# Performance work log

Hardware: AMD Instinct MI355X
Metric: run time of the kernel (lower is better)

The kernel has to match this reference:

```python
import jax, jax.numpy as jnp
import numpy as np

S = 1024          # num tokens (single prefill sequence)
H = 2880          # hidden_size
NH = 64           # num query heads
NKV = 8           # num kv heads
HD = 64           # head_dim
G = NH // NKV     # query heads per kv head
THETA = 10000.0
SCALE = HD ** -0.5


def _rope(x, positions):
    # neox-style rotary over full head_dim; x: [S, n_heads, HD]
    half = HD // 2
    inv_freq = 1.0 / (THETA ** (jnp.arange(half, dtype=jnp.float32) / half))
    ang = positions.astype(jnp.float32)[:, None] * inv_freq          # [S, half]
    cos = jnp.cos(ang)[:, None, :]
    sin = jnp.sin(ang)[:, None, :]
    x1, x2 = x[..., :half], x[..., half:]
    return jnp.concatenate([x1 * cos - x2 * sin, x2 * cos + x1 * sin], axis=-1)


def setup_inputs() -> dict:
    key = jax.random.key(0)
    k0, k1, k2, k3 = jax.random.split(key, 4)
    return {
        "positions": jnp.arange(S, dtype=jnp.int32),
        "hidden_states": jax.random.normal(k0, (S, H), dtype=jnp.float32),
        "qkv_w": jax.random.normal(k1, ((NH + 2 * NKV) * HD, H), dtype=jnp.float32) * 0.02,
        "o_w": jax.random.normal(k2, (H, NH * HD), dtype=jnp.float32) * 0.02,
        "sinks": jax.random.normal(k3, (NH,), dtype=jnp.float32),
    }


def reference(positions, hidden_states, qkv_w, o_w, sinks):
    # fused QKV projection (no bias, matching attention_bias=False)
    qkv = hidden_states @ qkv_w.T                                     # [S, 5120]
    q = qkv[:, : NH * HD].reshape(S, NH, HD)
    k = qkv[:, NH * HD : NH * HD + NKV * HD].reshape(S, NKV, HD)
    v = qkv[:, NH * HD + NKV * HD :].reshape(S, NKV, HD)

    # rotary on q and k (rotary_dim == head_dim)
    q = _rope(q, positions)
    k = _rope(k, positions)

    # GQA: group query heads by kv head -> [S, NKV, G, HD]
    qg = q.reshape(S, NKV, G, HD)

    logits = jnp.einsum("qghd,kgd->ghqk", qg, k) * SCALE              # [NKV, G, S, S]
    causal = positions[:, None] >= positions[None, :]                 # [S, S]
    logits = jnp.where(causal[None, None], logits, -jnp.inf)

    # attention sinks: per-head extra logit in the softmax denominator,
    # contributing no value vector.
    sink = sinks.reshape(NKV, G)[:, :, None, None]                    # [NKV, G, 1, 1]
    m = jnp.maximum(jnp.max(logits, axis=-1, keepdims=True), sink)
    p = jnp.exp(logits - m)                                           # [NKV, G, S, S]
    denom = jnp.sum(p, axis=-1, keepdims=True) + jnp.exp(sink - m)
    attn = jnp.einsum("ghqk,kgd->qghd", p / denom, v)                 # [S, NKV, G, HD]

    out = attn.reshape(S, NH * HD) @ o_w.T                            # [S, H]
    return out
```

## Files before the change

### kernel.cpp

```cpp
#include <hip/hip_runtime.h>
#include <hip/hip_bf16.h>
#include <math.h>

#define S_LEN 1024
#define HDIM  2880
#define NH    64
#define NKV   8
#define HD    64
#define QKV_N ((NH + 2*NKV) * HD)
#define O_K   (NH * HD)
#define SCALE 0.125f

typedef _Float16 f16x8 __attribute__((ext_vector_type(8)));
typedef _Float16 f16x4 __attribute__((ext_vector_type(4)));
typedef float    f32x4 __attribute__((ext_vector_type(4)));

__device__ __forceinline__ void cvt4(const float* __restrict__ s,
                                     _Float16* __restrict__ d, int i) {
    const float4 v = ((const float4*)s)[i];
    f16x4 p;
    p[0] = (_Float16)v.x; p[1] = (_Float16)v.y;
    p[2] = (_Float16)v.z; p[3] = (_Float16)v.w;
    ((f16x4*)d)[i] = p;
}

__global__ __launch_bounds__(256) void cvt_f32_f16(const float* __restrict__ src,
                                                   _Float16* __restrict__ dst, int n4) {
    const int stride = gridDim.x * blockDim.x;
    for (int i = blockIdx.x * blockDim.x + threadIdx.x; i < n4; i += stride)
        cvt4(src, dst, i);
}

__global__ __launch_bounds__(256) void cvt_all(const float* __restrict__ h,
                                               const float* __restrict__ qw,
                                               const float* __restrict__ ow,
                                               _Float16* __restrict__ dh,
                                               _Float16* __restrict__ dqw,
                                               _Float16* __restrict__ dow) {
    const int stride = gridDim.x * blockDim.x;
    const int t0 = blockIdx.x * blockDim.x + threadIdx.x;
    for (int i = t0; i < 737280;  i += stride) cvt4(h,  dh,  i);
    for (int i = t0; i < 3686400; i += stride) cvt4(qw, dqw, i);
    for (int i = t0; i < 2949120; i += stride) cvt4(ow, dow, i);
}

#define CSTR 68

#define DMA16(GP, LP) __builtin_amdgcn_global_load_lds( \
        (const __attribute__((address_space(1))) void*)(GP), \
        (__attribute__((address_space(3))) void*)(LP), 16, 0, 0)

template<typename CT>
__global__ __launch_bounds__(256) void gemm_ff(const _Float16* __restrict__ A,
                                               const _Float16* __restrict__ B,
                                               CT* __restrict__ C,
                                               int M, int N, int K) {
    __shared__ __align__(16) _Float16 sh[16384];

    const int tid  = threadIdx.x;
    const int lane = tid & 63;
    const int wave = tid >> 6;
    const int wr   = wave >> 1;
    const int wc   = wave & 1;
    const int quad = lane >> 4;
    const int fr   = lane & 15;
    const int ks   = quad * 8;
    const int row0 = blockIdx.y * 128;
    const int col0 = blockIdx.x * 128;

    const int klen   = K / (int)gridDim.z;
    const int kb     = (int)blockIdx.z * klen;
    const int nsteps = klen / 32;
    CT* Cp = C + (size_t)blockIdx.z * M * N;

    const int r0   = tid >> 2;
    const int ch   = (tid & 3) * 8;
    const int dst0 = (tid & ~63) * 8;

    const size_t aoff0 = (size_t)(row0 + r0)      * K;
    const size_t aoff1 = (size_t)(row0 + r0 + 64) * K;
    int bR0 = col0 + r0;      if (bR0 >= N) bR0 = N - 1;
    int bR1 = col0 + r0 + 64; if (bR1 >= N) bR1 = N - 1;
    const size_t boff0 = (size_t)bR0 * K;
    const size_t boff1 = (size_t)bR1 * K;

    f32x4 acc[4][4] = {};

    {
        const int kk = kb + ch;
        DMA16(A + aoff0 + kk, sh + dst0);
        DMA16(A + aoff1 + kk, sh + 2048 + dst0);
        DMA16(B + boff0 + kk, sh + 8192 + dst0);
        DMA16(B + boff1 + kk, sh + 8192 + 2048 + dst0);
    }

    for (int step = 0; step < nsteps; ++step) {
        const int cur = step & 1;
        _Float16* Acur = sh + cur * 4096;
        _Float16* Anxt = sh + (cur ^ 1) * 4096;
        _Float16* Bcur = sh + 8192 + cur * 4096;
        _Float16* Bnxt = sh + 8192 + (cur ^ 1) * 4096;

        __syncthreads();

        if (step + 1 < nsteps) {
            const int k1 = kb + (step + 1) * 32 + ch;
            DMA16(A + aoff0 + k1, Anxt + dst0);
            DMA16(A + aoff1 + k1, Anxt + 2048 + dst0);
            DMA16(B + boff0 + k1, Bnxt + dst0);
            DMA16(B + boff1 + k1, Bnxt + 2048 + dst0);
        }

        f16x8 af[4], bf[4];
#pragma unroll
        for (int mi = 0; mi < 4; ++mi)
            af[mi] = *(const f16x8*)&Acur[(wr * 64 + mi * 16 + fr) * 32 + ks];
#pragma unroll
        for (int ni = 0; ni < 4; ++ni)
            bf[ni] = *(const f16x8*)&Bcur[(wc * 64 + ni * 16 + fr) * 32 + ks];
#pragma unroll
        for (int mi = 0; mi < 4; ++mi)
#pragma unroll
            for (int ni = 0; ni < 4; ++ni)
                acc[mi][ni] = __builtin_amdgcn_mfma_f32_16x16x32_f16(
                    af[mi], bf[ni], acc[mi][ni], 0, 0, 0);
    }

#pragma unroll
    for (int p = 0; p < 2; ++p) {
        __syncthreads();
        if (wc == p) {
#pragma unroll
            for (int mi = 0; mi < 4; ++mi)
#pragma unroll
                for (int ni = 0; ni < 4; ++ni) {
                    const f32x4 v = acc[mi][ni];
#pragma unroll
                    for (int r = 0; r < 4; ++r)
                        sh[(wr * 64 + mi * 16 + quad * 4 + r) * CSTR + ni * 16 + fr] =
                            (_Float16)v[r];
                }
        }
        __syncthreads();
#pragma unroll
        for (int it = 0; it < 4; ++it) {
            const int id  = it * 256 + tid;
            const int row = id >> 3;
            const int chh = (id & 7) * 8;
            const int col = col0 + p * 64 + chh;
            if (col < N) {
                const f16x4 lo = *(const f16x4*)&sh[row * CSTR + chh];
                const f16x4 hi = *(const f16x4*)&sh[row * CSTR + chh + 4];
                if constexpr (sizeof(CT) == 2) {
                    f16x8 v;
                    v[0]=lo[0]; v[1]=lo[1]; v[2]=lo[2]; v[3]=lo[3];
                    v[4]=hi[0]; v[5]=hi[1]; v[6]=hi[2]; v[7]=hi[3];
                    *(f16x8*)&Cp[(size_t)(row0 + row) * N + col] = v;
                } else {
                    float4 v0 = make_float4((float)lo[0], (float)lo[1],
                                            (float)lo[2], (float)lo[3]);
                    float4 v1 = make_float4((float)hi[0], (float)hi[1],
                                            (float)hi[2], (float)hi[3]);
                    *(float4*)&Cp[(size_t)(row0 + row) * N + col]     = v0;
                    *(float4*)&Cp[(size_t)(row0 + row) * N + col + 4] = v1;
                }
            }
        }
    }
}

template<typename CT>
__global__ __launch_bounds__(256) void gemm_f16(const _Float16* __restrict__ A,
                                                const float* __restrict__ B,
                                                CT* __restrict__ C,
                                                int M, int N, int K) {
    __shared__ __align__(16) _Float16 sh[16384];

    const int tid  = threadIdx.x;
    const int lane = tid & 63;
    const int wave = tid >> 6;
    const int wr   = wave >> 1;
    const int wc   = wave & 1;
    const int quad = lane >> 4;
    const int fr   = lane & 15;
    const int ks   = quad * 8;
    const int row0 = blockIdx.y * 128;
    const int col0 = blockIdx.x * 128;

    const int klen   = K / (int)gridDim.z;
    const int kb     = (int)blockIdx.z * klen;
    const int nsteps = klen / 32;
    CT* Cp = C + (size_t)blockIdx.z * M * N;

    const int a_cbase0 = wave * 64;
    const int a_ci0 = a_cbase0 + lane;
    const int a_r0 = a_ci0 >> 2, a_ch0 = a_ci0 & 3;
    const int a_cbase1 = 256 + wave * 64;
    const int a_ci1 = a_cbase1 + lane;
    const int a_r1 = a_ci1 >> 2, a_ch1 = a_ci1 & 3;
    int b_r[4], b_ch[4];
#pragma unroll
    for (int it = 0; it < 4; ++it) {
        const int c4 = it * 256 + tid;
        b_r[it]  = c4 >> 3;
        b_ch[it] = (c4 & 7) << 2;
    }

    float4 breg[4];
    f32x4 acc[4][4] = {};

    {
        const _Float16* gp0 = A + (size_t)(row0 + a_r0) * K + kb + a_ch0 * 8;
        DMA16(gp0, sh + (size_t)a_cbase0 * 8);
        const _Float16* gp1 = A + (size_t)(row0 + a_r1) * K + kb + a_ch1 * 8;
        DMA16(gp1, sh + (size_t)a_cbase1 * 8);
#pragma unroll
        for (int it = 0; it < 4; ++it) {
            int brow = col0 + b_r[it];
            if (brow >= N) brow = N - 1;
            breg[it] = *(const float4*)&B[(size_t)brow * K + kb + b_ch[it]];
        }
        _Float16* Bs0 = sh + 8192;
#pragma unroll
        for (int it = 0; it < 4; ++it) {
            f16x4 p;
            p[0] = (_Float16)breg[it].x; p[1] = (_Float16)breg[it].y;
            p[2] = (_Float16)breg[it].z; p[3] = (_Float16)breg[it].w;
            *(f16x4*)&Bs0[b_r[it] * 32 + b_ch[it]] = p;
        }
    }

    for (int step = 0; step < nsteps; ++step) {
        const int cur = step & 1;
        const int nxt = cur ^ 1;
        _Float16* Acur = sh + cur * 4096;
        _Float16* Anxt = sh + nxt * 4096;
        _Float16* Bcur = sh + 8192 + cur * 4096;
        _Float16* Bnxt = sh + 8192 + nxt * 4096;

        __syncthreads();

        const bool more = (step + 1 < nsteps);
        if (more) {
            const int k1 = kb + (step + 1) * 32;
            const _Float16* gp0 = A + (size_t)(row0 + a_r0) * K + k1 + a_ch0 * 8;
            DMA16(gp0, Anxt + (size_t)a_cbase0 * 8);
            const _Float16* gp1 = A + (size_t)(row0 + a_r1) * K + k1 + a_ch1 * 8;
            DMA16(gp1, Anxt + (size_t)a_cbase1 * 8);
#pragma unroll
            for (int it = 0; it < 4; ++it) {
                int brow = col0 + b_r[it];
                if (brow >= N) brow = N - 1;
                breg[it] = *(const float4*)&B[(size_t)brow * K + k1 + b_ch[it]];
            }
        }

        f16x8 af[4], bfr[4];
#pragma unroll
        for (int mi = 0; mi < 4; ++mi)
            af[mi] = *(const f16x8*)&Acur[(wr * 64 + mi * 16 + fr) * 32 + ks];
#pragma unroll
        for (int ni = 0; ni < 4; ++ni)
            bfr[ni] = *(const f16x8*)&Bcur[(wc * 64 + ni * 16 + fr) * 32 + ks];
#pragma unroll
        for (int mi = 0; mi < 4; ++mi)
#pragma unroll
            for (int ni = 0; ni < 4; ++ni)
                acc[mi][ni] = __builtin_amdgcn_mfma_f32_16x16x32_f16(
                    af[mi], bfr[ni], acc[mi][ni], 0, 0, 0);

        if (more) {
#pragma unroll
            for (int it = 0; it < 4; ++it) {
                f16x4 p;
                p[0] = (_Float16)breg[it].x; p[1] = (_Float16)breg[it].y;
                p[2] = (_Float16)breg[it].z; p[3] = (_Float16)breg[it].w;
                *(f16x4*)&Bnxt[b_r[it] * 32 + b_ch[it]] = p;
            }
        }
    }

#pragma unroll
    for (int p = 0; p < 2; ++p) {
        __syncthreads();
        if (wc == p) {
#pragma unroll
            for (int mi = 0; mi < 4; ++mi)
#pragma unroll
                for (int ni = 0; ni < 4; ++ni) {
                    const f32x4 v = acc[mi][ni];
#pragma unroll
                    for (int r = 0; r < 4; ++r)
                        sh[(wr * 64 + mi * 16 + quad * 4 + r) * CSTR + ni * 16 + fr] =
                            (_Float16)v[r];
                }
        }
        __syncthreads();
#pragma unroll
        for (int it = 0; it < 4; ++it) {
            const int id  = it * 256 + tid;
            const int row = id >> 3;
            const int chh = (id & 7) * 8;
            const int col = col0 + p * 64 + chh;
            if (col < N) {
                const f16x4 lo = *(const f16x4*)&sh[row * CSTR + chh];
                const f16x4 hi = *(const f16x4*)&sh[row * CSTR + chh + 4];
                if constexpr (sizeof(CT) == 2) {
                    f16x8 v;
                    v[0]=lo[0]; v[1]=lo[1]; v[2]=lo[2]; v[3]=lo[3];
                    v[4]=hi[0]; v[5]=hi[1]; v[6]=hi[2]; v[7]=hi[3];
                    *(f16x8*)&Cp[(size_t)(row0 + row) * N + col] = v;
                } else {
                    float4 v0 = make_float4((float)lo[0], (float)lo[1],
                                            (float)lo[2], (float)lo[3]);
                    float4 v1 = make_float4((float)hi[0], (float)hi[1],
                                            (float)hi[2], (float)hi[3]);
                    *(float4*)&Cp[(size_t)(row0 + row) * N + col]     = v0;
                    *(float4*)&Cp[(size_t)(row0 + row) * N + col + 4] = v1;
                }
            }
        }
    }
}

__global__ __launch_bounds__(256) void rope_reduce(_Float16* __restrict__ parts,
                                                   int nsplit,
                                                   _Float16* __restrict__ vt,
                                                   const int* __restrict__ positions) {
    __shared__ float buf[QKV_N];
    const int s   = blockIdx.x;
    const int tid = threadIdx.x;
    const size_t PSTR = (size_t)S_LEN * QKV_N;

    for (int c = tid; c < QKV_N / 4; c += 256) {
        float4 a = make_float4(0.f, 0.f, 0.f, 0.f);
        for (int j = 0; j < nsplit; ++j) {
            const f16x4 v = ((const f16x4*)(parts + j * PSTR + (size_t)s * QKV_N))[c];
            a.x += (float)v[0]; a.y += (float)v[1];
            a.z += (float)v[2]; a.w += (float)v[3];
        }
        ((float4*)buf)[c] = a;
    }
    __syncthreads();

    const float pos = (float)positions[s];
    _Float16* orow = parts + (size_t)s * QKV_N;
    for (int w = tid; w < 72 * 32; w += 256) {
        const int h = w >> 5;
        const int t = w & 31;
        const float inv_freq = exp2f(-(float)t * (13.287712379549449f / 32.0f));
        const float ang = pos * inv_freq;
        float sn, cs;
        sincosf(ang, &sn, &cs);
        const float x1 = buf[h * 64 + t];
        const float x2 = buf[h * 64 + t + 32];
        orow[h * 64 + t]      = (_Float16)(x1 * cs - x2 * sn);
        orow[h * 64 + t + 32] = (_Float16)(x2 * cs + x1 * sn);
    }
    for (int c = tid; c < NKV * HD; c += 256)
        vt[(size_t)c * S_LEN + s] = (_Float16)buf[(NH + NKV) * HD + c];
}

__global__ __launch_bounds__(256) void o_reduce(const _Float16* __restrict__ parts,
                                                float* __restrict__ out,
                                                int n4, int nsplit) {
    const size_t PSTR = (size_t)S_LEN * HDIM;
    const int stride = gridDim.x * blockDim.x;
    for (int i = blockIdx.x * blockDim.x + threadIdx.x; i < n4; i += stride) {
        float4 a = make_float4(0.f, 0.f, 0.f, 0.f);
        for (int j = 0; j < nsplit; ++j) {
            const f16x4 v = ((const f16x4*)(parts + j * PSTR))[i];
            a.x += (float)v[0]; a.y += (float)v[1];
            a.z += (float)v[2]; a.w += (float)v[3];
        }
        ((float4*)out)[i] = a;
    }
}

#define LSTR 72
__global__ __launch_bounds__(256) void attn_mfma(const _Float16* __restrict__ qkv,
                                                 const _Float16* __restrict__ vt,
                                                 const float* __restrict__ sinks,
                                                 const int* __restrict__ positions,
                                                 _Float16* __restrict__ attn_out) {
    __shared__ __align__(16) _Float16 Ks[2][64 * LSTR];
    __shared__ __align__(16) _Float16 Vs[2][64 * LSTR];
    __shared__ __align__(16) _Float16 Ps[64 * LSTR];

    const int tid  = threadIdx.x;
    const int lane = tid & 63;
    const int wave = tid >> 6;
    const int fr   = lane & 15;
    const int quad = lane >> 4;
    const int ks8  = quad * 8;
    const int n    = blockIdx.x;
    const int qt   = (int)gridDim.y - 1 - (int)blockIdx.y;
    const int g    = n >> 3;

    int st_r[2], st_o[2];
#pragma unroll
    for (int it = 0; it < 2; ++it) {
        const int c = it * 256 + tid;
        st_r[it] = c >> 3;
        st_o[it] = (c & 7) * 8;
    }

    const _Float16* qrow = qkv + (size_t)(qt * 64 + wave * 16 + fr) * QKV_N + n * HD;
    const f16x8 a_q0 = *(const f16x8*)&qrow[ks8];
    const f16x8 a_q1 = *(const f16x8*)&qrow[32 + ks8];

    int pq[4];
#pragma unroll
    for (int r = 0; r < 4; ++r)
        pq[r] = positions[qt * 64 + wave * 16 + quad * 4 + r];

    const float sinkv = sinks[n];
    float m[4], l[4];
    f32x4 o[4] = {};
#pragma unroll
    for (int r = 0; r < 4; ++r) { m[r] = sinkv; l[r] = 1.0f; }

    f16x8 kreg[2], vreg[2];
    {
        const _Float16* Kg = qkv + (size_t)0 * QKV_N + NH * HD + g * HD;
        const _Float16* Vg = vt + (size_t)(g * HD) * S_LEN;
#pragma unroll
        for (int it = 0; it < 2; ++it) {
            kreg[it] = *(const f16x8*)&Kg[(size_t)st_r[it] * QKV_N + st_o[it]];
            vreg[it] = *(const f16x8*)&Vg[(size_t)st_r[it] * S_LEN + st_o[it]];
        }
#pragma unroll
        for (int it = 0; it < 2; ++it) {
            *(f16x8*)&Ks[0][st_r[it] * LSTR + st_o[it]] = kreg[it];
            *(f16x8*)&Vs[0][st_r[it] * LSTR + st_o[it]] = vreg[it];
        }
    }

    for (int kt = 0; kt <= qt; ++kt) {
        const int cur = kt & 1;
        const int nxt = cur ^ 1;
        __syncthreads();

        const bool more = (kt < qt);
        if (more) {
            const _Float16* Kg = qkv + (size_t)((kt + 1) * 64) * QKV_N + NH * HD + g * HD;
            const _Float16* Vg = vt + (size_t)(g * HD) * S_LEN + (kt + 1) * 64;
#pragma unroll
            for (int it = 0; it < 2; ++it) {
                kreg[it] = *(const f16x8*)&Kg[(size_t)st_r[it] * QKV_N + st_o[it]];
                vreg[it] = *(const f16x8*)&Vg[(size_t)st_r[it] * S_LEN + st_o[it]];
            }
        }

        f32x4 s[4] = {};
#pragma unroll
        for (int nt = 0; nt < 4; ++nt) {
            const f16x8 b0 = *(const f16x8*)&Ks[cur][(nt * 16 + fr) * LSTR + ks8];
            s[nt] = __builtin_amdgcn_mfma_f32_16x16x32_f16(a_q0, b0, s[nt], 0, 0, 0);
            const f16x8 b1 = *(const f16x8*)&Ks[cur][(nt * 16 + fr) * LSTR + 32 + ks8];
            s[nt] = __builtin_amdgcn_mfma_f32_16x16x32_f16(a_q1, b1, s[nt], 0, 0, 0);
        }

        const bool diag = (kt == qt);
        int pk[4];
        if (diag) {
#pragma unroll
            for (int nt = 0; nt < 4; ++nt) pk[nt] = positions[qt * 64 + nt * 16 + fr];
        }
#pragma unroll
        for (int nt = 0; nt < 4; ++nt)
#pragma unroll
            for (int r = 0; r < 4; ++r) {
                float sv = s[nt][r] * SCALE;
                if (diag && pk[nt] > pq[r]) sv = -3.0e38f;
                s[nt][r] = sv;
            }

#pragma unroll
        for (int r = 0; r < 4; ++r) {
            float tm = fmaxf(fmaxf(s[0][r], s[1][r]), fmaxf(s[2][r], s[3][r]));
            tm = fmaxf(tm, __shfl_xor(tm, 1, 64));
            tm = fmaxf(tm, __shfl_xor(tm, 2, 64));
            tm = fmaxf(tm, __shfl_xor(tm, 4, 64));
            tm = fmaxf(tm, __shfl_xor(tm, 8, 64));
            const float nm = fmaxf(m[r], tm);
            const float alpha = __expf(m[r] - nm);
            float rs = 0.0f;
#pragma unroll
            for (int nt = 0; nt < 4; ++nt) {
                const float p = __expf(s[nt][r] - nm);
                s[nt][r] = p;
                rs += p;
            }
            rs += __shfl_xor(rs, 1, 64);
            rs += __shfl_xor(rs, 2, 64);
            rs += __shfl_xor(rs, 4, 64);
            rs += __shfl_xor(rs, 8, 64);
            l[r] = l[r] * alpha + rs;
            m[r] = nm;
#pragma unroll
            for (int nt = 0; nt < 4; ++nt) o[nt][r] *= alpha;
        }

#pragma unroll
        for (int nt = 0; nt < 4; ++nt)
#pragma unroll
            for (int r = 0; r < 4; ++r)
                Ps[(wave * 16 + quad * 4 + r) * LSTR + nt * 16 + fr] = (_Float16)s[nt][r];
        __threadfence_block();

#pragma unroll
        for (int k2 = 0; k2 < 2; ++k2) {
            const f16x8 ap = *(const f16x8*)&Ps[(wave * 16 + fr) * LSTR + k2 * 32 + ks8];
#pragma unroll
            for (int nt = 0; nt < 4; ++nt) {
                const f16x8 bv = *(const f16x8*)&Vs[cur][(nt * 16 + fr) * LSTR + k2 * 32 + ks8];
                o[nt] = __builtin_amdgcn_mfma_f32_16x16x32_f16(ap, bv, o[nt], 0, 0, 0);
            }
        }

        if (more) {
#pragma unroll
            for (int it = 0; it < 2; ++it) {
                *(f16x8*)&Ks[nxt][st_r[it] * LSTR + st_o[it]] = kreg[it];
                *(f16x8*)&Vs[nxt][st_r[it] * LSTR + st_o[it]] = vreg[it];
            }
        }
    }

#pragma unroll
    for (int r = 0; r < 4; ++r) {
        const float inv = 1.0f / l[r];
        const size_t row = (size_t)(qt * 64 + wave * 16 + quad * 4 + r);
#pragma unroll
        for (int nt = 0; nt < 4; ++nt)
            attn_out[row * O_K + n * HD + nt * 16 + fr] = (_Float16)(o[nt][r] * inv);
    }
}

extern "C" void kernel_launch(void* const* d_in, const int* in_sizes, int n_in,
                              void* d_out, int out_size, void* d_ws, size_t ws_size,
                              hipStream_t stream) {
    const int*   positions = (const int*)d_in[0];
    const float* hidden    = (const float*)d_in[1];
    const float* qkv_w     = (const float*)d_in[2];
    const float* o_w       = (const float*)d_in[3];
    const float* sinks     = (const float*)d_in[4];
    float* out = (float*)d_out;

    const size_t n_hid  = (size_t)S_LEN * HDIM;
    const size_t n_qkv  = (size_t)S_LEN * QKV_N;
    const size_t n_attn = (size_t)S_LEN * O_K;
    const size_t n_vt   = (size_t)NKV * HD * S_LEN;
    const size_t n_out  = (size_t)S_LEN * HDIM;
    const size_t n_qw   = (size_t)QKV_N * HDIM;
    const size_t n_ow   = (size_t)HDIM * O_K;

    const int SP_Q = 3;
    const int SP_O = 4;

    const size_t need_full =
        (n_hid + SP_Q * n_qkv + n_attn + n_vt + n_qw + n_ow) * sizeof(_Float16);
    const size_t need_mid  = (n_hid + SP_Q * n_qkv + n_attn + n_vt) * sizeof(_Float16);

    if (ws_size >= need_full) {
        _Float16* hid_h  = (_Float16*)d_ws;
        _Float16* qkvp   = hid_h + n_hid;
        _Float16* attn_h = qkvp + SP_Q * n_qkv;
        _Float16* vt     = attn_h + n_attn;
        _Float16* qw_h   = vt + n_vt;
        _Float16* ow_h   = qw_h + n_qw;
        _Float16* opart  = qkvp;

        cvt_all<<<2048, 256, 0, stream>>>(hidden, qkv_w, o_w, hid_h, qw_h, ow_h);
        gemm_ff<_Float16><<<dim3(QKV_N / 128, S_LEN / 128, SP_Q), 256, 0, stream>>>(
            hid_h, qw_h, qkvp, S_LEN, QKV_N, HDIM);
        rope_reduce<<<S_LEN, 256, 0, stream>>>(qkvp, SP_Q, vt, positions);
        attn_mfma<<<dim3(NH, S_LEN / 64), 256, 0, stream>>>(qkvp, vt, sinks, positions, attn_h);
        gemm_ff<_Float16><<<dim3((HDIM + 127) / 128, S_LEN / 128, SP_O), 256, 0, stream>>>(
            attn_h, ow_h, opart, S_LEN, HDIM, O_K);
        o_reduce<<<1024, 256, 0, stream>>>(opart, out, (int)(n_out / 4), SP_O);
    } else if (ws_size >= need_mid) {
        _Float16* hid_h  = (_Float16*)d_ws;
        _Float16* qkvp   = hid_h + n_hid;
        _Float16* attn_h = qkvp + SP_Q * n_qkv;
        _Float16* vt     = attn_h + n_attn;
        _Float16* opart  = qkvp;

        cvt_f32_f16<<<512, 256, 0, stream>>>(hidden, hid_h, (int)(n_hid / 4));
        gemm_f16<_Float16><<<dim3(QKV_N / 128, S_LEN / 128, SP_Q), 256, 0, stream>>>(
            hid_h, qkv_w, qkvp, S_LEN, QKV_N, HDIM);
        rope_reduce<<<S_LEN, 256, 0, stream>>>(qkvp, SP_Q, vt, positions);
        attn_mfma<<<dim3(NH, S_LEN / 64), 256, 0, stream>>>(qkvp, vt, sinks, positions, attn_h);
        gemm_f16<_Float16><<<dim3((HDIM + 127) / 128, S_LEN / 128, SP_O), 256, 0, stream>>>(
            attn_h, o_w, opart, S_LEN, HDIM, O_K);
        o_reduce<<<1024, 256, 0, stream>>>(opart, out, (int)(n_out / 4), SP_O);
    } else {
        _Float16* hid_h  = (_Float16*)d_ws;
        _Float16* qkvp   = hid_h + n_hid;
        _Float16* attn_h = qkvp + n_qkv;
        _Float16* vt     = attn_h + n_attn;

        cvt_f32_f16<<<512, 256, 0, stream>>>(hidden, hid_h, (int)(n_hid / 4));
        gemm_f16<_Float16><<<dim3(QKV_N / 128, S_LEN / 128, 1), 256, 0, stream>>>(
            hid_h, qkv_w, qkvp, S_LEN, QKV_N, HDIM);
        rope_reduce<<<S_LEN, 256, 0, stream>>>(qkvp, 1, vt, positions);
        attn_mfma<<<dim3(NH, S_LEN / 64), 256, 0, stream>>>(qkvp, vt, sinks, positions, attn_h);
        gemm_f16<float><<<dim3((HDIM + 127) / 128, S_LEN / 128, 1), 256, 0, stream>>>(
            attn_h, o_w, out, S_LEN, HDIM, O_K);
    }
}
```

Measured before the change: 298.4 us.

## Add 256x256-tile eight-wave ping-pong GEMM for QKV and output projections

Introduces a new fp16 MFMA GEMM kernel with 256x256 block tiles and 512 threads. It uses direct global-to-LDS loads into double buffers with an XOR-swizzled layout, and interleaves quarter-tile MFMA phases with barriers and raised wave priority so that loads for the next K tile overlap compute. Both projection GEMMs in the full-workspace path now use it instead of the 128x128 kernel. The aim is more data reuse per block and fewer blocks. The cost is 128KB of LDS per block, which limits occupancy, and a grid of only a few hundred blocks, which may leave some CUs underused.

```diff
diff --git a/kernel.cpp b/kernel.cpp
--- a/kernel.cpp
+++ b/kernel.cpp
@@ -14,6 +14,15 @@
 typedef _Float16 f16x8 __attribute__((ext_vector_type(8)));
 typedef _Float16 f16x4 __attribute__((ext_vector_type(4)));
 typedef float    f32x4 __attribute__((ext_vector_type(4)));
+
+#define DMA16(GP, LP) __builtin_amdgcn_global_load_lds( \
+        (const __attribute__((address_space(1))) void*)(GP), \
+        (__attribute__((address_space(3))) void*)(LP), 16, 0, 0)
+
+#define BARRIER() __builtin_amdgcn_s_barrier()
+#define WAITV(n)  asm volatile("s_waitcnt vmcnt(" #n ")" ::: "memory")
+#define WAITL()   asm volatile("s_waitcnt lgkmcnt(0)" ::: "memory")
+#define SCHED0()  __builtin_amdgcn_sched_barrier(0)
 
 __device__ __forceinline__ void cvt4(const float* __restrict__ s,
                                      _Float16* __restrict__ d, int i) {
@@ -44,12 +53,177 @@
     for (int i = t0; i < 2949120; i += stride) cvt4(ow, dow, i);
 }
 
+__device__ __forceinline__ f16x8 lds_frag(const _Float16* base, int row, int kf) {
+    return *(const f16x8*)&base[row * 64 + (kf ^ ((row & 7) << 3))];
+}
+
+__device__ __forceinline__ void mfma_quad(f32x4 (&acc)[8][4], const f16x8 (&af)[4][2],
+                                          const f16x8 (&bf)[2][2], int mh, int nh) {
+    __builtin_amdgcn_s_setprio(1);
+#pragma unroll
+    for (int q4 = 0; q4 < 4; ++q4)
+#pragma unroll
+        for (int n2 = 0; n2 < 2; ++n2) {
+            f32x4 a = acc[mh * 4 + q4][nh * 2 + n2];
+            a = __builtin_amdgcn_mfma_f32_16x16x32_f16(af[q4][0], bf[n2][0], a, 0, 0, 0);
+            a = __builtin_amdgcn_mfma_f32_16x16x32_f16(af[q4][1], bf[n2][1], a, 0, 0, 0);
+            acc[mh * 4 + q4][nh * 2 + n2] = a;
+        }
+    __builtin_amdgcn_s_setprio(0);
+}
+
+__global__ __launch_bounds__(512, 2) void gemm_8p(const _Float16* __restrict__ A,
+                                                  const _Float16* __restrict__ B,
+                                                  _Float16* __restrict__ C,
+                                                  int M, int N, int K) {
+    __shared__ __align__(16) _Float16 sh[65536];
+
+    const int tid  = threadIdx.x;
+    const int lane = tid & 63;
+    const int wave = tid >> 6;
+    const int wr   = wave >> 2;
+    const int wc   = wave & 3;
+    const int quad = lane >> 4;
+    const int fr   = lane & 15;
+    const int row0 = blockIdx.y * 256;
+    const int col0 = blockIdx.x * 256;
+
+    const int klen = K / (int)gridDim.z;
+    const int kb   = (int)blockIdx.z * klen;
+    const int NT   = klen / 64;
+    _Float16* Cp = C + (size_t)blockIdx.z * M * N;
+
+    int    stDst[2];
+    size_t aOff[2][2], bOff[2][2];
+#pragma unroll
+    for (int r = 0; r < 2; ++r) {
+        const int c   = r * 512 + tid;
+        const int row = c >> 3;
+        const int sw  = ((c & 7) ^ (row & 7)) * 8;
+        stDst[r] = (c & ~63) * 8;
+#pragma unroll
+        for (int h = 0; h < 2; ++h) {
+            aOff[h][r] = (size_t)(row0 + h * 128 + row) * K + sw;
+            int br = col0 + h * 128 + row; if (br > N - 1) br = N - 1;
+            bOff[h][r] = (size_t)br * K + sw;
+        }
+    }
+    const _Float16* Ab = A + kb;
+    const _Float16* Bb = B + kb;
+
+#define STAGE2(GB, OFF, LB) do { \
+        DMA16((GB) + (OFF)[0], (LB) + stDst[0]); \
+        DMA16((GB) + (OFF)[1], (LB) + stDst[1]); } while (0)
+
+    f32x4 acc[8][4] = {};
+
+    STAGE2(Ab, aOff[0], sh);
+    STAGE2(Ab, aOff[1], sh + 8192);
+    STAGE2(Bb, bOff[0], sh + 32768);
+    STAGE2(Bb, bOff[1], sh + 32768 + 8192);
+    if (NT > 1) {
+        STAGE2(Ab + 64, aOff[0], sh + 16384);
+        STAGE2(Ab + 64, aOff[1], sh + 16384 + 8192);
+        WAITV(4);
+    } else {
+        WAITV(0);
+    }
+    BARRIER();
+
+    for (int t = 0; t < NT; ++t) {
+        _Float16* Ac = sh + ((t & 1) ? 16384 : 0);
+        _Float16* Bc = sh + 32768 + ((t & 1) ? 16384 : 0);
+        _Float16* Bn = sh + 32768 + ((t & 1) ? 0 : 16384);
+        const bool st1 = (t + 1 < NT);
+        const bool st2 = (t + 2 < NT);
+        const int  k1  = (t + 1) * 64;
+        const int  k2  = (t + 2) * 64;
+
+        f16x8 aF0[4][2], aF1[4][2], bF[2][2];
+
+#pragma unroll
+        for (int q4 = 0; q4 < 4; ++q4) {
+            const int row = wr * 128 + q4 * 16 + fr;
+            aF0[q4][0] = lds_frag(Ac, row, quad * 8);
+            aF0[q4][1] = lds_frag(Ac, row, 32 + quad * 8);
+        }
+#pragma unroll
+        for (int n2 = 0; n2 < 2; ++n2) {
+            const int row = wc * 64 + n2 * 16 + fr;
+            bF[n2][0] = lds_frag(Bc, row, quad * 8);
+            bF[n2][1] = lds_frag(Bc, row, 32 + quad * 8);
+        }
+        if (st1) STAGE2(Bb + k1, bOff[0], Bn);
+        BARRIER(); WAITL(); SCHED0();
+        mfma_quad(acc, aF0, bF, 0, 0);
+        BARRIER();
+
+#pragma unroll
+        for (int q4 = 0; q4 < 4; ++q4) {
+            const int row = wr * 128 + 64 + q4 * 16 + fr;
+            aF1[q4][0] = lds_frag(Ac, row, quad * 8);
+            aF1[q4][1] = lds_frag(Ac, row, 32 + quad * 8);
+        }
+        if (st1) STAGE2(Bb + k1, bOff[1], Bn + 8192);
+        BARRIER(); WAITL(); SCHED0();
+        mfma_quad(acc, aF1, bF, 1, 0);
+        BARRIER();
+
+#pragma unroll
+        for (int n2 = 0; n2 < 2; ++n2) {
+            const int row = wc * 64 + 32 + n2 * 16 + fr;
+            bF[n2][0] = lds_frag(Bc, row, quad * 8);
+            bF[n2][1] = lds_frag(Bc, row, 32 + quad * 8);
+        }
+        if (st2) STAGE2(Ab + k2, aOff[0], Ac);
+        BARRIER(); WAITL(); SCHED0();
+        mfma_quad(acc, aF1, bF, 1, 1);
+        BARRIER();
+
+        if (st2) {
+            STAGE2(Ab + k2, aOff[1], Ac + 8192);
+            WAITV(4);
+        } else {
+            WAITV(0);
+        }
+        BARRIER(); WAITL(); SCHED0();
+        mfma_quad(acc, aF0, bF, 0, 1);
+        BARRIER();
+    }
+
+    __syncthreads();
+    _Float16* cbuf = sh;
+#pragma unroll
+    for (int h = 0; h < 2; ++h) {
+        if (wr == h) {
+#pragma unroll
+            for (int mi = 0; mi < 8; ++mi)
+#pragma unroll
+                for (int ni = 0; ni < 4; ++ni) {
+                    const f32x4 v = acc[mi][ni];
+#pragma unroll
+                    for (int rr = 0; rr < 4; ++rr)
+                        cbuf[(mi * 16 + quad * 4 + rr) * 264 + wc * 64 + ni * 16 + fr] =
+                            (_Float16)v[rr];
+                }
+        }
+        __syncthreads();
+#pragma unroll
+        for (int u = 0; u < 8; ++u) {
+            const int c    = u * 512 + tid;
+            const int rowL = c >> 5;
+            const int ch   = (c & 31) * 8;
+            const int col  = col0 + ch;
+            if (col < N)
+                *(f16x8*)&Cp[(size_t)(row0 + h * 128 + rowL) * N + col] =
+                    *(const f16x8*)&cbuf[rowL * 264 + ch];
+        }
+        __syncthreads();
+    }
+#undef STAGE2
+}
+
 #define CSTR 68
-
-#define DMA16(GP, LP) __builtin_amdgcn_global_load_lds( \
-        (const __attribute__((address_space(1))) void*)(GP), \
-        (__attribute__((address_space(3))) void*)(LP), 16, 0, 0)
-
 template<typename CT>
 __global__ __launch_bounds__(256) void gemm_ff(const _Float16* __restrict__ A,
                                                const _Float16* __restrict__ B,
@@ -573,11 +747,11 @@
         _Float16* opart  = qkvp;
 
         cvt_all<<<2048, 256, 0, stream>>>(hidden, qkv_w, o_w, hid_h, qw_h, ow_h);
-        gemm_ff<_Float16><<<dim3(QKV_N / 128, S_LEN / 128, SP_Q), 256, 0, stream>>>(
+        gemm_8p<<<dim3(QKV_N / 256, S_LEN / 256, SP_Q), 512, 0, stream>>>(
             hid_h, qw_h, qkvp, S_LEN, QKV_N, HDIM);
         rope_reduce<<<S_LEN, 256, 0, stream>>>(qkvp, SP_Q, vt, positions);
         attn_mfma<<<dim3(NH, S_LEN / 64), 256, 0, stream>>>(qkvp, vt, sinks, positions, attn_h);
-        gemm_ff<_Float16><<<dim3((HDIM + 127) / 128, S_LEN / 128, SP_O), 256, 0, stream>>>(
+        gemm_8p<<<dim3((HDIM + 255) / 256, S_LEN / 256, SP_O), 512, 0, stream>>>(
             attn_h, ow_h, opart, S_LEN, HDIM, O_K);
         o_reduce<<<1024, 256, 0, stream>>>(opart, out, (int)(n_out / 4), SP_O);
     } else if (ws_size >= need_mid) {
```

Result: faster. 268.5 us (-10.0%).
